# Kernel optimization log

Hardware: AMD Instinct MI355X
Metric: run time of the kernel (lower is better)

## Reference

```python
import jax, jax.numpy as jnp
import numpy as np

# PCEN constants (from __init__ defaults)
ALPHA = 0.98
DELTA = 2.0
R = 0.5
S = 0.025
EPS = 1e-6


def setup_inputs() -> dict:
    key = jax.random.key(0)
    # mel spectrogram energies: [batch, mel_bins, time], nonnegative
    x = jax.random.uniform(key, (64, 128, 4096), dtype=jnp.float32)
    return {"x": x}


def _ema_smooth(x):
    # x: [B, C, T]. smooth[0] = x[0]; smooth[t] = (1-S)*smooth[t-1] + S*x[t]
    x_t = jnp.moveaxis(x, -1, 0)  # [T, B, C]
    init = x_t[0]

    def step(carry, xt):
        sm = (1.0 - S) * carry + S * xt
        return sm, sm

    _, rest = jax.lax.scan(step, init, x_t[1:])  # [T-1, B, C]
    smooth = jnp.concatenate([init[None], rest], axis=0)  # [T, B, C]
    return jnp.moveaxis(smooth, 0, -1)  # [B, C, T]


def reference(x):
    smooth = _ema_smooth(x)
    return (x / (smooth + EPS) ** ALPHA + DELTA) ** R - DELTA ** R
```

## Files before the change

kernel.cpp:

```cpp
#include <hip/hip_runtime.h>
#include <math.h>


#define T_LEN 4096
#define BLOCK 1024
#define PER   4
#define NWAVE (BLOCK / 64)

__global__ __launch_bounds__(BLOCK) void pcen_kernel(const float* __restrict__ x,
                                                     float* __restrict__ out) {
    constexpr float A_COEF = 0.975f;
    constexpr float S_COEF = 0.025f;
    constexpr float ALPHA  = 0.98f;
    constexpr float EPS    = 1e-6f;
    constexpr float DELTA  = 2.0f;
    constexpr float SQRT_DELTA = 1.4142135623730951f;

    const int row = blockIdx.x;
    const float* __restrict__ xr  = x   + (size_t)row * T_LEN;
    float* __restrict__       orr = out + (size_t)row * T_LEN;

    const int tid  = threadIdx.x;
    const int base = tid * PER;

    float xv[PER];
    {
        float4 v = *(const float4*)(xr + base);
        xv[0] = v.x; xv[1] = v.y; xv[2] = v.z; xv[3] = v.w;
    }

    float A, B;
    if (tid == 0) {
        A = 0.0f; B = xv[0];
        for (int i = 1; i < PER; ++i) { B = fmaf(A_COEF, B, S_COEF * xv[i]); }
    } else {
        A = A_COEF; B = S_COEF * xv[0];
#pragma unroll
        for (int i = 1; i < PER; ++i) {
            B = fmaf(A_COEF, B, S_COEF * xv[i]);
            A = A * A_COEF;
        }
    }

    const int lane = tid & 63;
#pragma unroll
    for (int off = 1; off < 64; off <<= 1) {
        float Au = __shfl_up(A, off);
        float Bu = __shfl_up(B, off);
        if (lane >= off) {
            B = fmaf(A, Bu, B);
            A = A * Au;
        }
    }

    __shared__ float wA[NWAVE], wB[NWAVE];
    const int wid = tid >> 6;
    if (lane == 63) { wA[wid] = A; wB[wid] = B; }
    __syncthreads();

    float Aex = __shfl_up(A, 1);
    float Bex = __shfl_up(B, 1);
    if (lane == 0) { Aex = 1.0f; Bex = 0.0f; }

    float WB = 0.0f;
    for (int w = 0; w < wid; ++w) {
        WB = fmaf(wA[w], WB, wB[w]);
    }

    float y = fmaf(Aex, WB, Bex);

    float ov[PER];
#pragma unroll
    for (int i = 0; i < PER; ++i) {
        if (tid == 0 && i == 0) y = xv[0];
        else                    y = fmaf(A_COEF, y, S_COEF * xv[i]);
        float p = __builtin_amdgcn_exp2f(-ALPHA * __builtin_amdgcn_logf(y + EPS));
        ov[i] = __builtin_amdgcn_sqrtf(fmaf(xv[i], p, DELTA)) - SQRT_DELTA;
    }

    float4 v;
    v.x = ov[0]; v.y = ov[1]; v.z = ov[2]; v.w = ov[3];
    *(float4*)(orr + base) = v;
}

extern "C" void kernel_launch(void* const* d_in, const int* in_sizes, int n_in,
                              void* d_out, int out_size, void* d_ws, size_t ws_size,
                              hipStream_t stream) {
    const float* x = (const float*)d_in[0];
    float* out = (float*)d_out;
    const int rows = in_sizes[0] / T_LEN;
    pcen_kernel<<<rows, BLOCK, 0, stream>>>(x, out);
}
```

Measured before the change: 222.1 us.

## Scan each row within a single wavefront, removing block-level sync and LDS

Maps one 4096-sample row to one 64-lane wavefront instead of a 1024-thread block. Each lane processes 16 float4 chunks, doing a scan within the wave using constant power coefficients and carrying the prefix across chunks with readlane. This removes the shared-memory round trip, the __syncthreads and the serial per-wave combine loop. In exchange each lane keeps 16 float4 values in registers, which raises register pressure, and the grid shrinks to rows/4 blocks of 256 threads, lowering parallelism.

```diff
diff --git a/kernel.cpp b/kernel.cpp
--- a/kernel.cpp
+++ b/kernel.cpp
@@ -3,84 +3,112 @@
 
 
 #define T_LEN 4096
-#define BLOCK 1024
-#define PER   4
-#define NWAVE (BLOCK / 64)
+#define BLOCK 256
+#define NSUB  16
 
-__global__ __launch_bounds__(BLOCK) void pcen_kernel(const float* __restrict__ x,
-                                                     float* __restrict__ out) {
+constexpr double dpow(double b, int n) {
+    double r = 1.0;
+    for (int i = 0; i < n; ++i) r *= b;
+    return r;
+}
+
+__global__ __launch_bounds__(BLOCK, 4) void pcen_kernel(const float* __restrict__ x,
+                                                        float* __restrict__ out) {
     constexpr float A_COEF = 0.975f;
     constexpr float S_COEF = 0.025f;
     constexpr float ALPHA  = 0.98f;
     constexpr float EPS    = 1e-6f;
     constexpr float DELTA  = 2.0f;
     constexpr float SQRT_DELTA = 1.4142135623730951f;
+    constexpr float CS0 = (float)dpow(0.975, 4);
+    constexpr float CS1 = (float)dpow(0.975, 8);
+    constexpr float CS2 = (float)dpow(0.975, 16);
+    constexpr float CS3 = (float)dpow(0.975, 32);
+    constexpr float CS4 = (float)dpow(0.975, 64);
+    constexpr float CS5 = (float)dpow(0.975, 128);
+    constexpr float A256 = (float)dpow(0.975, 256);
+    constexpr float AP1 = (float)dpow(0.975, 1);
+    constexpr float AP2 = (float)dpow(0.975, 2);
+    constexpr float AP3 = (float)dpow(0.975, 3);
+    constexpr float AP4 = (float)dpow(0.975, 4);
 
-    const int row = blockIdx.x;
+    const int tid  = threadIdx.x;
+    const int lane = tid & 63;
+    const int wid  = tid >> 6;
+    const int row  = blockIdx.x * 4 + wid;
+
     const float* __restrict__ xr  = x   + (size_t)row * T_LEN;
     float* __restrict__       orr = out + (size_t)row * T_LEN;
 
-    const int tid  = threadIdx.x;
-    const int base = tid * PER;
+    float a4l = 1.0f;
+    a4l *= (lane & 1)  ? CS0 : 1.0f;
+    a4l *= (lane & 2)  ? CS1 : 1.0f;
+    a4l *= (lane & 4)  ? CS2 : 1.0f;
+    a4l *= (lane & 8)  ? CS3 : 1.0f;
+    a4l *= (lane & 16) ? CS4 : 1.0f;
+    a4l *= (lane & 32) ? CS5 : 1.0f;
 
-    float xv[PER];
-    {
-        float4 v = *(const float4*)(xr + base);
-        xv[0] = v.x; xv[1] = v.y; xv[2] = v.z; xv[3] = v.w;
+    float4 xq[NSUB];
+#pragma unroll
+    for (int s = 0; s < NSUB; ++s)
+        xq[s] = *(const float4*)(xr + 256 * s + 4 * lane);
+
+    float Bs[NSUB];
+#pragma unroll
+    for (int s = 0; s < NSUB; ++s) {
+        float b = (s == 0 && lane == 0) ? xq[s].x : S_COEF * xq[s].x;
+        b = fmaf(A_COEF, b, S_COEF * xq[s].y);
+        b = fmaf(A_COEF, b, S_COEF * xq[s].z);
+        b = fmaf(A_COEF, b, S_COEF * xq[s].w);
+        float bu;
+        bu = __shfl_up(b, 1);  if (lane >= 1)  b = fmaf(CS0, bu, b);
+        bu = __shfl_up(b, 2);  if (lane >= 2)  b = fmaf(CS1, bu, b);
+        bu = __shfl_up(b, 4);  if (lane >= 4)  b = fmaf(CS2, bu, b);
+        bu = __shfl_up(b, 8);  if (lane >= 8)  b = fmaf(CS3, bu, b);
+        bu = __shfl_up(b, 16); if (lane >= 16) b = fmaf(CS4, bu, b);
+        bu = __shfl_up(b, 32); if (lane >= 32) b = fmaf(CS5, bu, b);
+        Bs[s] = b;
     }
 
-    float A, B;
-    if (tid == 0) {
-        A = 0.0f; B = xv[0];
-        for (int i = 1; i < PER; ++i) { B = fmaf(A_COEF, B, S_COEF * xv[i]); }
-    } else {
-        A = A_COEF; B = S_COEF * xv[0];
+    float y = 0.0f;
 #pragma unroll
-        for (int i = 1; i < PER; ++i) {
-            B = fmaf(A_COEF, B, S_COEF * xv[i]);
-            A = A * A_COEF;
+    for (int s = 0; s < NSUB; ++s) {
+        float bex = __shfl_up(Bs[s], 1);
+        if (lane == 0) bex = 0.0f;
+        float yl = fmaf(a4l, y, bex);
+
+        float bi0 = (s == 0 && lane == 0) ? xq[s].x : S_COEF * xq[s].x;
+        float bi1 = fmaf(A_COEF, bi0, S_COEF * xq[s].y);
+        float bi2 = fmaf(A_COEF, bi1, S_COEF * xq[s].z);
+        float bi3 = fmaf(A_COEF, bi2, S_COEF * xq[s].w);
+
+        float sm0 = fmaf(AP1, yl, bi0);
+        float sm1 = fmaf(AP2, yl, bi1);
+        float sm2 = fmaf(AP3, yl, bi2);
+        float sm3 = fmaf(AP4, yl, bi3);
+
+        float4 o;
+        {
+            float p = __builtin_amdgcn_exp2f(-ALPHA * __builtin_amdgcn_logf(sm0 + EPS));
+            o.x = __builtin_amdgcn_sqrtf(fmaf(xq[s].x, p, DELTA)) - SQRT_DELTA;
         }
+        {
+            float p = __builtin_amdgcn_exp2f(-ALPHA * __builtin_amdgcn_logf(sm1 + EPS));
+            o.y = __builtin_amdgcn_sqrtf(fmaf(xq[s].y, p, DELTA)) - SQRT_DELTA;
+        }
+        {
+            float p = __builtin_amdgcn_exp2f(-ALPHA * __builtin_amdgcn_logf(sm2 + EPS));
+            o.z = __builtin_amdgcn_sqrtf(fmaf(xq[s].z, p, DELTA)) - SQRT_DELTA;
+        }
+        {
+            float p = __builtin_amdgcn_exp2f(-ALPHA * __builtin_amdgcn_logf(sm3 + EPS));
+            o.w = __builtin_amdgcn_sqrtf(fmaf(xq[s].w, p, DELTA)) - SQRT_DELTA;
+        }
+        *(float4*)(orr + 256 * s + 4 * lane) = o;
+
+        y = fmaf(A256, y,
+                 __uint_as_float(__builtin_amdgcn_readlane(__float_as_uint(Bs[s]), 63)));
     }
-
-    const int lane = tid & 63;
-#pragma unroll
-    for (int off = 1; off < 64; off <<= 1) {
-        float Au = __shfl_up(A, off);
-        float Bu = __shfl_up(B, off);
-        if (lane >= off) {
-            B = fmaf(A, Bu, B);
-            A = A * Au;
-        }
-    }
-
-    __shared__ float wA[NWAVE], wB[NWAVE];
-    const int wid = tid >> 6;
-    if (lane == 63) { wA[wid] = A; wB[wid] = B; }
-    __syncthreads();
-
-    float Aex = __shfl_up(A, 1);
-    float Bex = __shfl_up(B, 1);
-    if (lane == 0) { Aex = 1.0f; Bex = 0.0f; }
-
-    float WB = 0.0f;
-    for (int w = 0; w < wid; ++w) {
-        WB = fmaf(wA[w], WB, wB[w]);
-    }
-
-    float y = fmaf(Aex, WB, Bex);
-
-    float ov[PER];
-#pragma unroll
-    for (int i = 0; i < PER; ++i) {
-        if (tid == 0 && i == 0) y = xv[0];
-        else                    y = fmaf(A_COEF, y, S_COEF * xv[i]);
-        float p = __builtin_amdgcn_exp2f(-ALPHA * __builtin_amdgcn_logf(y + EPS));
-        ov[i] = __builtin_amdgcn_sqrtf(fmaf(xv[i], p, DELTA)) - SQRT_DELTA;
-    }
-
-    float4 v;
-    v.x = ov[0]; v.y = ov[1]; v.z = ov[2]; v.w = ov[3];
-    *(float4*)(orr + base) = v;
 }
 
 extern "C" void kernel_launch(void* const* d_in, const int* in_sizes, int n_in,
@@ -89,5 +117,5 @@
     const float* x = (const float*)d_in[0];
     float* out = (float*)d_out;
     const int rows = in_sizes[0] / T_LEN;
-    pcen_kernel<<<rows, BLOCK, 0, stream>>>(x, out);
+    pcen_kernel<<<rows / 4, BLOCK, 0, stream>>>(x, out);
 }
```

Result: slower. 232.4 us (+4.6%).
